# Kernel tuning notes

Measured on AMD Instinct MI355X. Metric: run time of the kernel, lower is better.

Reference implementation:

```python
import jax, jax.numpy as jnp
import numpy as np

N = 50000   # nodes
E = 800000  # edges (avg degree 16)
F = 64      # num_features (channels per irrep)
R = 8       # radial basis size
H = 64      # radial MLP hidden
S = 10      # num_species
NPATH = 5   # tensor-product paths: s*Y0->0, s*Y1->1, v*Y0->1, v.Y1->0, v x Y1->1
AVG_NEIGH = 16.0


def setup_inputs() -> dict:
    key = jax.random.key(0)
    ks = jax.random.split(key, 20)
    def w(k, shape, fan_in):
        return jax.random.normal(k, shape, dtype=jnp.float32) / np.sqrt(fan_in)
    return dict(
        vectors=jax.random.normal(ks[0], (E, 3), dtype=jnp.float32),
        node_feats_s=jax.random.normal(ks[1], (N, F), dtype=jnp.float32),
        node_feats_v=jax.random.normal(ks[2], (N, F, 3), dtype=jnp.float32),
        radial_embedding=jax.random.normal(ks[3], (E, R), dtype=jnp.float32),
        Wu_s=w(ks[7], (F, F), F), Wu_v=w(ks[8], (F, F), F),
        W_r1=w(ks[9], (R, H), R), W_r2=w(ks[10], (H, NPATH * F), H),
        Wd_s=w(ks[11], (F, F), F), Wd_v=w(ks[12], (F, F), F),
        w_sym_s=jax.random.normal(ks[13], (S, 3, F), dtype=jnp.float32),
        w_sym_v=jax.random.normal(ks[14], (S, 2, F), dtype=jnp.float32),
        WL_s=w(ks[15], (F, F), F), WL_v=w(ks[16], (F, F), F),
        W_skip_s=w(ks[17], (S, F, F), F), W_skip_v=w(ks[18], (S, F, F), F),
        W_out=w(ks[19], (F, 1), F),
        node_specie=jax.random.randint(ks[4], (N,), 0, S),
        senders=jax.random.randint(ks[5], (E,), 0, N),
        receivers=jax.random.randint(ks[6], (E,), 0, N),
    )


def reference(vectors, node_feats_s, node_feats_v, radial_embedding,
              Wu_s, Wu_v, W_r1, W_r2, Wd_s, Wd_v,
              w_sym_s, w_sym_v, WL_s, WL_v, W_skip_s, W_skip_v, W_out,
              node_specie, senders, receivers):
    n = node_feats_s.shape[0]
    # ---- self-connection: species-indexed linear (skip_tp), per-irrep channel mix
    sc_s = jnp.einsum('nf,nfg->ng', node_feats_s, W_skip_s[node_specie])
    sc_v = jnp.einsum('nfc,nfg->ngc', node_feats_v, W_skip_v[node_specie])
    # ---- InteractionBlock: linear up
    s = node_feats_s @ Wu_s                                  # [N,F]
    v = jnp.einsum('nfc,fg->ngc', node_feats_v, Wu_v)        # [N,F,3]
    # radial MLP -> per-edge, per-path, per-channel tensor-product weights
    h = jax.nn.silu(radial_embedding @ W_r1)
    w = (h @ W_r2).reshape(-1, NPATH, s.shape[1])            # [E,5,F]
    # spherical harmonics (l=1): unit edge vectors
    Y1 = vectors / (jnp.linalg.norm(vectors, axis=-1, keepdims=True) + 1e-9)  # [E,3]
    xs = s[senders]                                          # [E,F]
    xv = v[senders]                                          # [E,F,3]
    # CG tensor product paths (0e+1o) x (Y0+Y1) -> 0e + 1o
    m_s = w[:, 0] * xs + w[:, 3] * jnp.einsum('efc,ec->ef', xv, Y1)
    m_v = (w[:, 1, :, None] * xs[:, :, None] * Y1[:, None, :]
           + w[:, 2, :, None] * xv
           + w[:, 4, :, None] * jnp.cross(xv, Y1[:, None, :]))
    # scatter-sum aggregation over receivers
    agg_s = jax.ops.segment_sum(m_s, receivers, num_segments=n)
    agg_v = jax.ops.segment_sum(m_v, receivers, num_segments=n)
    # linear down to num_features * interaction_irreps
    s = agg_s @ Wd_s
    v = jnp.einsum('nfc,fg->ngc', agg_v, Wd_v)
    # epsilon is None -> divide by sqrt(avg_num_neighbors)
    inv = 1.0 / np.sqrt(AVG_NEIGH).astype(np.float32)
    s = s * inv
    v = v * inv
    # ---- EquivariantProductBasisBlock: symmetric contraction (correlation=2),
    # species-indexed per-channel weights over the symmetric CG basis
    ws = w_sym_s[node_specie]                                # [N,3,F]
    wv = w_sym_v[node_specie]                                # [N,2,F]
    ps = ws[:, 0] * s + ws[:, 1] * s * s + ws[:, 2] * jnp.sum(v * v, axis=-1)
    pv = wv[:, 0, :, None] * v + wv[:, 1, :, None] * (s[:, :, None] * v)
    # linear to num_features * hidden_irreps
    fs = ps @ WL_s
    fv = jnp.einsum('nfc,fg->ngc', pv, WL_v)
    # residual skip connection
    fs = fs + sc_s
    fv = fv + sc_v
    # ---- LinearReadoutBlock to output_irreps = '0e'
    node_outputs = fs @ W_out                                # [N,1]
    return node_outputs, fs, fv
```

## Files before the change

kernel.cpp:

```cpp
#include <hip/hip_runtime.h>
#include <stdint.h>

#define F 64
#define RDIM 8
#define HDIM 64
#define NPATH 5
#define EB 64
#define PADH 72
#define PADN 324
#define NSP 16
#define PB 72
#define NT 4

typedef _Float16 half8 __attribute__((ext_vector_type(8)));
typedef _Float16 half4 __attribute__((ext_vector_type(4)));
typedef float floatx4 __attribute__((ext_vector_type(4)));

__device__ inline half8 h8_from_f32(const float* p) {
    float4 a = ((const float4*)p)[0];
    float4 b = ((const float4*)p)[1];
    half8 h;
    h[0] = (_Float16)a.x; h[1] = (_Float16)a.y; h[2] = (_Float16)a.z; h[3] = (_Float16)a.w;
    h[4] = (_Float16)b.x; h[5] = (_Float16)b.y; h[6] = (_Float16)b.z; h[7] = (_Float16)b.w;
    return h;
}

__device__ inline half8 h8_from_f32_stride3(const float* p) {
    half8 h;
#pragma unroll
    for (int j = 0; j < 8; ++j) h[j] = (_Float16)p[j * 3];
    return h;
}

__device__ inline half8 h8_zero() {
    half8 h;
#pragma unroll
    for (int j = 0; j < 8; ++j) h[j] = (_Float16)0.f;
    return h;
}

__global__ __launch_bounds__(256) void k_pre_mfma(
    const float* __restrict__ nfs, const float* __restrict__ nfv,
    const float* __restrict__ Wus, const float* __restrict__ Wuv,
    half4* __restrict__ comb, int N)
{
    __shared__ _Float16 BT[2][64 * PB];
    const int tid = threadIdx.x;
    const int wave = tid >> 6, lane = tid & 63;
    const int l15 = lane & 15, lq = lane >> 4;
    const int tb0 = blockIdx.x * 64;

    {
        const float* srcs[2] = { Wus, Wuv };
#pragma unroll
        for (int m = 0; m < 2; ++m) {
            const float* W = srcs[m];
#pragma unroll
            for (int rep = 0; rep < 16; ++rep) {
                int id = rep * 256 + tid;
                int k = id >> 6, n = id & 63;
                BT[m][n * PB + k] = (_Float16)W[k * F + n];
            }
        }
    }
    __syncthreads();

    const int tb = tb0 + wave * 16;
    const int ndA = tb + l15;

#define BFRAG(m, nt, ks) (*(const half8*)&BT[m][((nt) * 16 + l15) * PB + (ks) * 32 + lq * 8])

    floatx4 c[4][NT];
#pragma unroll
    for (int q = 0; q < 4; ++q)
#pragma unroll
        for (int nt = 0; nt < NT; ++nt) c[q][nt] = (floatx4){0.f, 0.f, 0.f, 0.f};

#pragma unroll
    for (int ks = 0; ks < 2; ++ks) {
        half8 a_s, a_v0, a_v1, a_v2;
        if (ndA < N) {
            a_s  = h8_from_f32(nfs + (size_t)ndA * F + ks * 32 + lq * 8);
            const float* vb = nfv + ((size_t)ndA * F + ks * 32 + lq * 8) * 3;
            a_v0 = h8_from_f32_stride3(vb + 0);
            a_v1 = h8_from_f32_stride3(vb + 1);
            a_v2 = h8_from_f32_stride3(vb + 2);
        } else {
            a_s = a_v0 = a_v1 = a_v2 = h8_zero();
        }
#pragma unroll
        for (int nt = 0; nt < NT; ++nt) {
            half8 bs = BFRAG(0, nt, ks);
            half8 bv = BFRAG(1, nt, ks);
            c[0][nt] = __builtin_amdgcn_mfma_f32_16x16x32_f16(a_s,  bs, c[0][nt], 0, 0, 0);
            c[1][nt] = __builtin_amdgcn_mfma_f32_16x16x32_f16(a_v0, bv, c[1][nt], 0, 0, 0);
            c[2][nt] = __builtin_amdgcn_mfma_f32_16x16x32_f16(a_v1, bv, c[2][nt], 0, 0, 0);
            c[3][nt] = __builtin_amdgcn_mfma_f32_16x16x32_f16(a_v2, bv, c[3][nt], 0, 0, 0);
        }
    }
#undef BFRAG

#pragma unroll
    for (int r = 0; r < 4; ++r) {
        const int nd = tb + lq * 4 + r;
        if (nd < N) {
#pragma unroll
            for (int nt = 0; nt < NT; ++nt) {
                half4 o;
                o[0] = (_Float16)c[0][nt][r];
                o[1] = (_Float16)c[1][nt][r];
                o[2] = (_Float16)c[2][nt][r];
                o[3] = (_Float16)c[3][nt][r];
                comb[(size_t)nd * F + nt * 16 + l15] = o;
            }
        }
    }
}

__global__ __launch_bounds__(256) void k_hist(
    const int* __restrict__ recv, int* __restrict__ cnt, int E,
    const int* __restrict__ specie, int* __restrict__ nbin, int N)
{
    __shared__ int lbin[NSP];
    const int tid = threadIdx.x;
    if (tid < NSP) lbin[tid] = 0;
    __syncthreads();
    const int i0 = blockIdx.x * 256 + tid;
    const int stride = gridDim.x * 256;
    for (int e = i0; e < E; e += stride) atomicAdd(&cnt[recv[e]], 1);
    for (int n = i0; n < N; n += stride) atomicAdd(&lbin[specie[n]], 1);
    __syncthreads();
    if (tid < NSP && lbin[tid] > 0) atomicAdd(&nbin[tid], lbin[tid]);
}

__global__ __launch_bounds__(1024) void k_scanA(
    const int* __restrict__ cnt, int* __restrict__ bsum, int N)
{
    __shared__ int lsum[1024];
    const int tid = threadIdx.x;
    const int i = blockIdx.x * 1024 + tid;
    int x = (i < N) ? cnt[i] : 0;
    lsum[tid] = x;
    __syncthreads();
    for (int off = 512; off > 0; off >>= 1) {
        if (tid < off) lsum[tid] += lsum[tid + off];
        __syncthreads();
    }
    if (tid == 0) bsum[blockIdx.x] = lsum[0];
}

__global__ __launch_bounds__(64) void k_scanB(
    int* __restrict__ bsum, int nb,
    const int* __restrict__ nbin, int* __restrict__ ncur)
{
    const int lane = threadIdx.x;
    int carry = 0;
    for (int base = 0; base < nb; base += 64) {
        const int idx = base + lane;
        int v = (idx < nb) ? bsum[idx] : 0;
        int incl = v;
#pragma unroll
        for (int off = 1; off < 64; off <<= 1) {
            int u = __shfl_up(incl, off, 64);
            if (lane >= off) incl += u;
        }
        int tot = __shfl(incl, 63, 64);
        if (idx < nb) bsum[idx] = incl - v + carry;
        carry += tot;
    }
    if (lane == 0) {
        int run = 0;
        for (int s = 0; s < NSP; ++s) {
            ncur[s] = run;
            run += ((nbin[s] + 63) >> 6) << 6;
        }
    }
}

__global__ __launch_bounds__(1024) void k_scanC(
    const int* __restrict__ cnt, const int* __restrict__ bsum,
    int* __restrict__ cursor, int N)
{
    __shared__ int lsum[1024];
    const int tid = threadIdx.x;
    const int i = blockIdx.x * 1024 + tid;
    int x = (i < N) ? cnt[i] : 0;
    lsum[tid] = x;
    __syncthreads();
    int acc = x;
    for (int off = 1; off < 1024; off <<= 1) {
        int add = (tid >= off) ? lsum[tid - off] : 0;
        __syncthreads();
        acc += add;
        lsum[tid] = acc;
        __syncthreads();
    }
    if (i < N) cursor[i] = acc - x + bsum[blockIdx.x];
}

__global__ __launch_bounds__(256) void k_scatter(
    const int* __restrict__ recv, const int* __restrict__ send,
    int* __restrict__ cursor, int* __restrict__ perm,
    int2* __restrict__ srsort, int E,
    const int* __restrict__ specie, int* __restrict__ ncur,
    int* __restrict__ nperm, int N)
{
    __shared__ int lbin[NSP], lbase[NSP], lcur[NSP];
    const int tid = threadIdx.x;
    const int i0 = blockIdx.x * 256 + tid;
    const int stride = gridDim.x * 256;
    for (int e = i0; e < E; e += stride) {
        int r = recv[e];
        int p = atomicAdd(&cursor[r], 1);
        perm[p] = e;
        srsort[p] = make_int2(send[e], r);
    }
    if (tid < NSP) { lbin[tid] = 0; lcur[tid] = 0; }
    __syncthreads();
    int sp = -1;
    if (i0 < N) { sp = specie[i0]; atomicAdd(&lbin[sp], 1); }
    __syncthreads();
    if (tid < NSP && lbin[tid] > 0) lbase[tid] = atomicAdd(&ncur[tid], lbin[tid]);
    __syncthreads();
    if (i0 < N) {
        int off = atomicAdd(&lcur[sp], 1);
        nperm[lbase[sp] + off] = i0;
    }
}

__global__ __launch_bounds__(256, 3) void k_edge(
    const float* __restrict__ vecs, const float* __restrict__ re,
    const float* __restrict__ Wr1, const float* __restrict__ Wr2,
    const int* __restrict__ perm, const int2* __restrict__ srsort,
    const half4* __restrict__ comb,
    float* __restrict__ agg_s, float* __restrict__ agg_v, int E)
{
    __shared__ _Float16 h_lds[EB * PADH];
    __shared__ _Float16 w_lds[EB * PADN];
    const int tid = threadIdx.x;
    const int wave = tid >> 6, lane = tid & 63;
    const int l15 = lane & 15, lq = lane >> 4;

    half8 bfrag[5][2];
#pragma unroll
    for (int nt = 0; nt < 5; ++nt)
#pragma unroll
        for (int ks = 0; ks < 2; ++ks)
#pragma unroll
            for (int j = 0; j < 8; ++j) {
                int k = ks * 32 + lq * 8 + j;
                int n = wave * 80 + nt * 16 + l15;
                bfrag[nt][ks][j] = (_Float16)Wr2[k * (NPATH * F) + n];
            }

    float w1r[RDIM];
#pragma unroll
    for (int r = 0; r < RDIM; ++r) w1r[r] = Wr1[r * HDIM + lane];

    const int niter = (E + EB - 1) / EB;
    for (int it = blockIdx.x; it < niter; it += gridDim.x) {
        const int base = it * EB;
        const bool full = (base + EB <= E);

        if (full) {
            const int ew = base + wave * 16;
            int pm[16];
#pragma unroll
            for (int j = 0; j < 4; ++j)
                ((int4*)pm)[j] = ((const int4*)(perm + ew))[j];
            float4 ra[4], rb[4];
#pragma unroll
            for (int j = 0; j < 4; ++j) {
                const float4* rp = (const float4*)(re + (size_t)pm[j] * RDIM);
                ra[j] = rp[0]; rb[j] = rp[1];
            }
#pragma unroll
            for (int t = 0; t < 16; ++t) {
                float4 A = ra[t & 3], B = rb[t & 3];
                if (t < 12) {
                    const float4* rp = (const float4*)(re + (size_t)pm[t + 4] * RDIM);
                    ra[t & 3] = rp[0]; rb[t & 3] = rp[1];
                }
                float h = A.x * w1r[0] + A.y * w1r[1] + A.z * w1r[2] + A.w * w1r[3]
                        + B.x * w1r[4] + B.y * w1r[5] + B.z * w1r[6] + B.w * w1r[7];
                h = h / (1.f + __expf(-h));
                h_lds[(wave * 16 + t) * PADH + lane] = (_Float16)h;
            }
        } else {
            for (int t = 0; t < 16; ++t) {
                const int eloc = wave * 16 + t;
                const int e = base + eloc;
                float h = 0.f;
                if (e < E) {
                    const int pe = perm[e];
                    const float4* rp = (const float4*)(re + (size_t)pe * RDIM);
                    float4 A = rp[0], B = rp[1];
                    h = A.x * w1r[0] + A.y * w1r[1] + A.z * w1r[2] + A.w * w1r[3]
                      + B.x * w1r[4] + B.y * w1r[5] + B.z * w1r[6] + B.w * w1r[7];
                    h = h / (1.f + __expf(-h));
                }
                h_lds[eloc * PADH + lane] = (_Float16)h;
            }
        }
        __syncthreads();

        floatx4 c[4][5];
#pragma unroll
        for (int mt = 0; mt < 4; ++mt)
#pragma unroll
            for (int nt = 0; nt < 5; ++nt)
                c[mt][nt] = (floatx4){0.f, 0.f, 0.f, 0.f};
#pragma unroll
        for (int ks = 0; ks < 2; ++ks) {
            half8 a[4];
#pragma unroll
            for (int mt = 0; mt < 4; ++mt)
                a[mt] = *(const half8*)&h_lds[(mt * 16 + l15) * PADH + ks * 32 + lq * 8];
#pragma unroll
            for (int mt = 0; mt < 4; ++mt)
#pragma unroll
                for (int nt = 0; nt < 5; ++nt)
                    c[mt][nt] = __builtin_amdgcn_mfma_f32_16x16x32_f16(
                        a[mt], bfrag[nt][ks], c[mt][nt], 0, 0, 0);
        }
#pragma unroll
        for (int mt = 0; mt < 4; ++mt)
#pragma unroll
            for (int nt = 0; nt < 5; ++nt)
#pragma unroll
                for (int r = 0; r < 4; ++r) {
                    int row = mt * 16 + lq * 4 + r;
                    int col = wave * 80 + nt * 16 + l15;
                    w_lds[row * PADN + col] = (_Float16)c[mt][nt][r];
                }
        __syncthreads();

        if (full) {
            const int ew = base + wave * 16;
            int pm[16];
            int2 sr[16];
#pragma unroll
            for (int j = 0; j < 4; ++j)
                ((int4*)pm)[j] = ((const int4*)(perm + ew))[j];
#pragma unroll
            for (int j = 0; j < 8; ++j)
                ((int4*)sr)[j] = ((const int4*)(srsort + ew))[j];
            half4 gb[4];
            float vxr[4], vyr[4], vzr[4];
#pragma unroll
            for (int j = 0; j < 4; ++j) {
                gb[j] = comb[(size_t)sr[j].x * F + lane];
                const float* vp = vecs + (size_t)pm[j] * 3;
                vxr[j] = vp[0]; vyr[j] = vp[1]; vzr[j] = vp[2];
            }
            float accs = 0.f, acc0 = 0.f, acc1 = 0.f, acc2 = 0.f;
            int cur = sr[0].y;
#pragma unroll
            for (int t = 0; t < 16; ++t) {
                half4 g = gb[t & 3];
                float vx = vxr[t & 3], vy = vyr[t & 3], vz = vzr[t & 3];
                if (t < 12) {
                    gb[t & 3] = comb[(size_t)sr[t + 4].x * F + lane];
                    const float* vp = vecs + (size_t)pm[t + 4] * 3;
                    vxr[t & 3] = vp[0]; vyr[t & 3] = vp[1]; vzr[t & 3] = vp[2];
                }
                const int eloc = wave * 16 + t;
                float nrm = sqrtf(vx * vx + vy * vy + vz * vz);
                float inv = 1.f / (nrm + 1e-9f);
                float Yx = vx * inv, Yy = vy * inv, Yz = vz * inv;
                float w0  = (float)w_lds[eloc * PADN + 0 * F + lane];
                float w1p = (float)w_lds[eloc * PADN + 1 * F + lane];
                float w2p = (float)w_lds[eloc * PADN + 2 * F + lane];
                float w3p = (float)w_lds[eloc * PADN + 3 * F + lane];
                float w4p = (float)w_lds[eloc * PADN + 4 * F + lane];
                float xs = (float)g[0], x0 = (float)g[1], x1 = (float)g[2], x2 = (float)g[3];
                float dvY = x0 * Yx + x1 * Yy + x2 * Yz;
                float ms = w0 * xs + w3p * dvY;
                float m0 = w1p * xs * Yx + w2p * x0 + w4p * (x1 * Yz - x2 * Yy);
                float m1 = w1p * xs * Yy + w2p * x1 + w4p * (x2 * Yx - x0 * Yz);
                float m2 = w1p * xs * Yz + w2p * x2 + w4p * (x0 * Yy - x1 * Yx);
                if (sr[t].y != cur) {
                    float* asb = agg_s + (size_t)cur * F;
                    float* avb = agg_v + (size_t)cur * 3 * F;
                    unsafeAtomicAdd(&asb[lane], accs);
                    unsafeAtomicAdd(&avb[lane], acc0);
                    unsafeAtomicAdd(&avb[F + lane], acc1);
                    unsafeAtomicAdd(&avb[2 * F + lane], acc2);
                    accs = acc0 = acc1 = acc2 = 0.f;
                    cur = sr[t].y;
                }
                accs += ms; acc0 += m0; acc1 += m1; acc2 += m2;
            }
            {
                float* asb = agg_s + (size_t)cur * F;
                float* avb = agg_v + (size_t)cur * 3 * F;
                unsafeAtomicAdd(&asb[lane], accs);
                unsafeAtomicAdd(&avb[lane], acc0);
                unsafeAtomicAdd(&avb[F + lane], acc1);
                unsafeAtomicAdd(&avb[2 * F + lane], acc2);
            }
        } else {
            for (int t = 0; t < 16; ++t) {
                const int eloc = wave * 16 + t;
                const int e = base + eloc;
                if (e >= E) break;
                const int pe = perm[e];
                const int2 sr = srsort[e];
                const int snd = sr.x, rcv = sr.y;
                const float* vp = vecs + (size_t)pe * 3;
                float vx = vp[0], vy = vp[1], vz = vp[2];
                float nrm = sqrtf(vx * vx + vy * vy + vz * vz);
                float inv = 1.f / (nrm + 1e-9f);
                float Yx = vx * inv, Yy = vy * inv, Yz = vz * inv;
                half4 g = comb[(size_t)snd * F + lane];
                float w0  = (float)w_lds[eloc * PADN + 0 * F + lane];
                float w1p = (float)w_lds[eloc * PADN + 1 * F + lane];
                float w2p = (float)w_lds[eloc * PADN + 2 * F + lane];
                float w3p = (float)w_lds[eloc * PADN + 3 * F + lane];
                float w4p = (float)w_lds[eloc * PADN + 4 * F + lane];
                float xs = (float)g[0], x0 = (float)g[1], x1 = (float)g[2], x2 = (float)g[3];
                float dvY = x0 * Yx + x1 * Yy + x2 * Yz;
                float ms = w0 * xs + w3p * dvY;
                float m0 = w1p * xs * Yx + w2p * x0 + w4p * (x1 * Yz - x2 * Yy);
                float m1 = w1p * xs * Yy + w2p * x1 + w4p * (x2 * Yx - x0 * Yz);
                float m2 = w1p * xs * Yz + w2p * x2 + w4p * (x0 * Yy - x1 * Yx);
                float* asb = agg_s + (size_t)rcv * F;
                float* avb = agg_v + (size_t)rcv * 3 * F;
                unsafeAtomicAdd(&asb[lane], ms);
                unsafeAtomicAdd(&avb[lane], m0);
                unsafeAtomicAdd(&avb[F + lane], m1);
                unsafeAtomicAdd(&avb[2 * F + lane], m2);
            }
        }
    }
}

__global__ __launch_bounds__(256) void k_post_mfma(
    const float* __restrict__ agg_s, const float* __restrict__ agg_v,
    const float* __restrict__ nfs, const float* __restrict__ nfv,
    const float* __restrict__ Wds, const float* __restrict__ Wdv,
    const float* __restrict__ wss, const float* __restrict__ wsv,
    const float* __restrict__ WLs, const float* __restrict__ WLv,
    const float* __restrict__ Wsks, const float* __restrict__ Wskv,
    const float* __restrict__ Wout, const int* __restrict__ specie,
    const int* __restrict__ nperm,
    float* __restrict__ out0, float* __restrict__ out_fs,
    float* __restrict__ out_fv, int N)
{
    __shared__ _Float16 BT[6][64 * PB];
    __shared__ _Float16 P_lds[4][16 * PB];
    const int tid = threadIdx.x;
    const int wave = tid >> 6, lane = tid & 63;
    const int l15 = lane & 15, lq = lane >> 4;
    const int tb0 = blockIdx.x * 64;

    const int nfirst = nperm[tb0];
    const int sp = (nfirst < 0) ? 0 : specie[nfirst];

    {
        const float* srcs[6] = { Wds, Wdv,
                                 Wsks + (size_t)sp * F * F, Wskv + (size_t)sp * F * F,
                                 WLs, WLv };
#pragma unroll
        for (int m = 0; m < 6; ++m) {
            const float* W = srcs[m];
#pragma unroll
            for (int rep = 0; rep < 16; ++rep) {
                int id = rep * 256 + tid;
                int k = id >> 6, n = id & 63;
                BT[m][n * PB + k] = (_Float16)W[k * F + n];
            }
        }
    }
    __syncthreads();

    const int tb = tb0 + wave * 16;
    const int ndA = nperm[tb + l15];
    int ndr[4];
#pragma unroll
    for (int r = 0; r < 4; ++r) ndr[r] = nperm[tb + lq * 4 + r];

#define BFRAG(m, nt, ks) (*(const half8*)&BT[m][((nt) * 16 + l15) * PB + (ks) * 32 + lq * 8])

    floatx4 csk[4][NT];
#pragma unroll
    for (int q = 0; q < 4; ++q)
#pragma unroll
        for (int nt = 0; nt < NT; ++nt) csk[q][nt] = (floatx4){0.f, 0.f, 0.f, 0.f};
#pragma unroll
    for (int ks = 0; ks < 2; ++ks) {
        half8 a_s, a_v0, a_v1, a_v2;
        if (ndA >= 0) {
            a_s  = h8_from_f32(nfs + (size_t)ndA * F + ks * 32 + lq * 8);
            const float* vb = nfv + ((size_t)ndA * F + ks * 32 + lq * 8) * 3;
            a_v0 = h8_from_f32_stride3(vb + 0);
            a_v1 = h8_from_f32_stride3(vb + 1);
            a_v2 = h8_from_f32_stride3(vb + 2);
        } else {
            a_s = a_v0 = a_v1 = a_v2 = h8_zero();
        }
#pragma unroll
        for (int nt = 0; nt < NT; ++nt) {
            half8 bs = BFRAG(2, nt, ks);
            half8 bv = BFRAG(3, nt, ks);
            csk[0][nt] = __builtin_amdgcn_mfma_f32_16x16x32_f16(a_s,  bs, csk[0][nt], 0, 0, 0);
            csk[1][nt] = __builtin_amdgcn_mfma_f32_16x16x32_f16(a_v0, bv, csk[1][nt], 0, 0, 0);
            csk[2][nt] = __builtin_amdgcn_mfma_f32_16x16x32_f16(a_v1, bv, csk[2][nt], 0, 0, 0);
            csk[3][nt] = __builtin_amdgcn_mfma_f32_16x16x32_f16(a_v2, bv, csk[3][nt], 0, 0, 0);
        }
    }

    floatx4 cdn[4][NT];
#pragma unroll
    for (int q = 0; q < 4; ++q)
#pragma unroll
        for (int nt = 0; nt < NT; ++nt) cdn[q][nt] = (floatx4){0.f, 0.f, 0.f, 0.f};
#pragma unroll
    for (int ks = 0; ks < 2; ++ks) {
        half8 a_s, a_v0, a_v1, a_v2;
        if (ndA >= 0) {
            a_s  = h8_from_f32(agg_s + (size_t)ndA * F + ks * 32 + lq * 8);
            const float* vb = agg_v + (size_t)ndA * 3 * F + ks * 32 + lq * 8;
            a_v0 = h8_from_f32(vb);
            a_v1 = h8_from_f32(vb + F);
            a_v2 = h8_from_f32(vb + 2 * F);
        } else {
            a_s = a_v0 = a_v1 = a_v2 = h8_zero();
        }
#pragma unroll
        for (int nt = 0; nt < NT; ++nt) {
            half8 bs = BFRAG(0, nt, ks);
            half8 bv = BFRAG(1, nt, ks);
            cdn[0][nt] = __builtin_amdgcn_mfma_f32_16x16x32_f16(a_s,  bs, cdn[0][nt], 0, 0, 0);
            cdn[1][nt] = __builtin_amdgcn_mfma_f32_16x16x32_f16(a_v0, bv, cdn[1][nt], 0, 0, 0);
            cdn[2][nt] = __builtin_amdgcn_mfma_f32_16x16x32_f16(a_v1, bv, cdn[2][nt], 0, 0, 0);
            cdn[3][nt] = __builtin_amdgcn_mfma_f32_16x16x32_f16(a_v2, bv, cdn[3][nt], 0, 0, 0);
        }
    }

#pragma unroll
    for (int nt = 0; nt < NT; ++nt) {
        const int g = nt * 16 + l15;
        float a0 = wss[(sp * 3 + 0) * F + g];
        float a1 = wss[(sp * 3 + 1) * F + g];
        float a2 = wss[(sp * 3 + 2) * F + g];
        float b0 = wsv[(sp * 2 + 0) * F + g];
        float b1 = wsv[(sp * 2 + 1) * F + g];
#pragma unroll
        for (int r = 0; r < 4; ++r) {
            const float inv = 0.25f;
            float s2  = cdn[0][nt][r] * inv;
            float v20 = cdn[1][nt][r] * inv;
            float v21 = cdn[2][nt][r] * inv;
            float v22 = cdn[3][nt][r] * inv;
            cdn[0][nt][r] = a0 * s2 + a1 * s2 * s2
                          + a2 * (v20 * v20 + v21 * v21 + v22 * v22);
            cdn[1][nt][r] = b0 * v20 + b1 * s2 * v20;
            cdn[2][nt][r] = b0 * v21 + b1 * s2 * v21;
            cdn[3][nt][r] = b0 * v22 + b1 * s2 * v22;
        }
    }

#pragma unroll
    for (int q = 0; q < 4; ++q) {
#pragma unroll
        for (int nt = 0; nt < NT; ++nt)
#pragma unroll
            for (int r = 0; r < 4; ++r)
                P_lds[wave][(lq * 4 + r) * PB + nt * 16 + l15] = (_Float16)cdn[q][nt][r];
        __syncthreads();
        half8 ap0 = *(const half8*)&P_lds[wave][l15 * PB + 0 * 32 + lq * 8];
        half8 ap1 = *(const half8*)&P_lds[wave][l15 * PB + 1 * 32 + lq * 8];
        const int bm = (q == 0) ? 4 : 5;
#pragma unroll
        for (int nt = 0; nt < NT; ++nt) {
            csk[q][nt] = __builtin_amdgcn_mfma_f32_16x16x32_f16(ap0, BFRAG(bm, nt, 0), csk[q][nt], 0, 0, 0);
            csk[q][nt] = __builtin_amdgcn_mfma_f32_16x16x32_f16(ap1, BFRAG(bm, nt, 1), csk[q][nt], 0, 0, 0);
        }
        __syncthreads();
    }
#undef BFRAG

    float wo[NT];
#pragma unroll
    for (int nt = 0; nt < NT; ++nt) wo[nt] = Wout[nt * 16 + l15];
#pragma unroll
    for (int r = 0; r < 4; ++r) {
        const int nd = ndr[r];
        float po = 0.f;
        if (nd >= 0) {
#pragma unroll
            for (int nt = 0; nt < NT; ++nt) {
                const int g = nt * 16 + l15;
                float fs = csk[0][nt][r];
                out_fs[(size_t)nd * F + g] = fs;
                po += fs * wo[nt];
                float* fvp = out_fv + ((size_t)nd * F + g) * 3;
                fvp[0] = csk[1][nt][r];
                fvp[1] = csk[2][nt][r];
                fvp[2] = csk[3][nt][r];
            }
            po += __shfl_xor(po, 1, 64);
            po += __shfl_xor(po, 2, 64);
            po += __shfl_xor(po, 4, 64);
            po += __shfl_xor(po, 8, 64);
            if (l15 == 0) out0[nd] = po;
        }
    }
}

extern "C" void kernel_launch(void* const* d_in, const int* in_sizes, int n_in,
                              void* d_out, int out_size, void* d_ws, size_t ws_size,
                              hipStream_t stream)
{
    const float* vectors = (const float*)d_in[0];
    const float* nfs  = (const float*)d_in[1];
    const float* nfv  = (const float*)d_in[2];
    const float* re   = (const float*)d_in[3];
    const float* Wus  = (const float*)d_in[4];
    const float* Wuv  = (const float*)d_in[5];
    const float* Wr1  = (const float*)d_in[6];
    const float* Wr2  = (const float*)d_in[7];
    const float* Wds  = (const float*)d_in[8];
    const float* Wdv  = (const float*)d_in[9];
    const float* wss  = (const float*)d_in[10];
    const float* wsv  = (const float*)d_in[11];
    const float* WLs  = (const float*)d_in[12];
    const float* WLv  = (const float*)d_in[13];
    const float* Wsks = (const float*)d_in[14];
    const float* Wskv = (const float*)d_in[15];
    const float* Wout = (const float*)d_in[16];
    const int* specie    = (const int*)d_in[17];
    const int* senders   = (const int*)d_in[18];
    const int* receivers = (const int*)d_in[19];

    const int N = in_sizes[1] / F;
    const int E = in_sizes[18];

    const size_t NF = (size_t)N * F;
    const int NPAD_MAX = N + NSP * 64 + 64;
    half4* comb  = (half4*)d_ws;
    float* agg_s = (float*)((char*)d_ws + NF * sizeof(half4));
    float* agg_v = agg_s + NF;
    int*   perm  = (int*)(agg_v + 3 * NF);
    int2*  srsort = (int2*)(perm + E);
    int*   cnt    = (int*)(srsort + E);
    int*   nbin   = cnt + N;
    int*   ncur   = nbin + NSP;
    int*   cursor = ncur + NSP;
    int*   bsum   = cursor + N;
    int*   nperm  = bsum + 64;

    hipMemsetAsync(agg_s, 0, (size_t)4 * NF * sizeof(float), stream);
    hipMemsetAsync(cnt, 0, (size_t)(N + NSP) * sizeof(int), stream);
    hipMemsetAsync(nperm, 0xFF, (size_t)NPAD_MAX * sizeof(int), stream);

    const int nb64 = (N + 63) / 64;
    const int nbs = (N + 1023) / 1024;
    const int nbp = (N + NSP * 64 + 63) / 64;

    k_pre_mfma<<<nb64, 256, 0, stream>>>(nfs, nfv, Wus, Wuv, comb, N);
    k_hist<<<1024, 256, 0, stream>>>(receivers, cnt, E, specie, nbin, N);
    k_scanA<<<nbs, 1024, 0, stream>>>(cnt, bsum, N);
    k_scanB<<<1, 64, 0, stream>>>(bsum, nbs, nbin, ncur);
    k_scanC<<<nbs, 1024, 0, stream>>>(cnt, bsum, cursor, N);
    k_scatter<<<1024, 256, 0, stream>>>(receivers, senders, cursor,
                                        perm, srsort, E, specie, ncur, nperm, N);
    k_edge<<<2048, 256, 0, stream>>>(vectors, re, Wr1, Wr2, perm, srsort,
                                     comb, agg_s, agg_v, E);
    float* out0   = (float*)d_out;
    float* out_fs = out0 + N;
    float* out_fv = out_fs + (size_t)N * F;
    k_post_mfma<<<nbp, 256, 0, stream>>>(agg_s, agg_v, nfs, nfv, Wds, Wdv,
                                         wss, wsv, WLs, WLv, Wsks, Wskv,
                                         Wout, specie, nperm,
                                         out0, out_fs, out_fv, N);
}
```

Before: 551.9 us.

## Halve edge block size, pack sorted edge metadata into int4, raise occupancy

Edge tiles shrink from 64 to 32 edges per block (8 per wave), which cuts LDS use and accumulator registers so the launch bound can rise from 3 to 6 blocks per CU. The separate perm and sender/receiver arrays are merged into a single 16-byte record per edge, written with a nontemporal store and read once into registers, which removes the duplicate index loads. The grid grows to 2500 blocks. In exchange the MFMA work per barrier halves, the prefetch depth per wave is shorter, and runs of the same receiver split more often, so there may be more atomics.

```diff
diff --git a/kernel.cpp b/kernel.cpp
--- a/kernel.cpp
+++ b/kernel.cpp
@@ -5,7 +5,8 @@
 #define RDIM 8
 #define HDIM 64
 #define NPATH 5
-#define EB 64
+#define EB 32
+#define EPW 8
 #define PADH 72
 #define PADN 324
 #define NSP 16
@@ -15,6 +16,7 @@
 typedef _Float16 half8 __attribute__((ext_vector_type(8)));
 typedef _Float16 half4 __attribute__((ext_vector_type(4)));
 typedef float floatx4 __attribute__((ext_vector_type(4)));
+typedef int intx4 __attribute__((ext_vector_type(4)));
 
 __device__ inline half8 h8_from_f32(const float* p) {
     float4 a = ((const float4*)p)[0];
@@ -200,8 +202,7 @@
 
 __global__ __launch_bounds__(256) void k_scatter(
     const int* __restrict__ recv, const int* __restrict__ send,
-    int* __restrict__ cursor, int* __restrict__ perm,
-    int2* __restrict__ srsort, int E,
+    int* __restrict__ cursor, intx4* __restrict__ esort, int E,
     const int* __restrict__ specie, int* __restrict__ ncur,
     int* __restrict__ nperm, int N)
 {
@@ -212,8 +213,8 @@
     for (int e = i0; e < E; e += stride) {
         int r = recv[e];
         int p = atomicAdd(&cursor[r], 1);
-        perm[p] = e;
-        srsort[p] = make_int2(send[e], r);
+        intx4 v = (intx4){e, send[e], r, 0};
+        __builtin_nontemporal_store(v, &esort[p]);
     }
     if (tid < NSP) { lbin[tid] = 0; lcur[tid] = 0; }
     __syncthreads();
@@ -228,10 +229,10 @@
     }
 }
 
-__global__ __launch_bounds__(256, 3) void k_edge(
+__global__ __launch_bounds__(256, 6) void k_edge(
     const float* __restrict__ vecs, const float* __restrict__ re,
     const float* __restrict__ Wr1, const float* __restrict__ Wr2,
-    const int* __restrict__ perm, const int2* __restrict__ srsort,
+    const intx4* __restrict__ esort,
     const half4* __restrict__ comb,
     float* __restrict__ agg_s, float* __restrict__ agg_v, int E)
 {
@@ -261,38 +262,37 @@
     for (int it = blockIdx.x; it < niter; it += gridDim.x) {
         const int base = it * EB;
         const bool full = (base + EB <= E);
+        intx4 es[EPW];
 
         if (full) {
-            const int ew = base + wave * 16;
-            int pm[16];
-#pragma unroll
-            for (int j = 0; j < 4; ++j)
-                ((int4*)pm)[j] = ((const int4*)(perm + ew))[j];
+            const int ew = base + wave * EPW;
+#pragma unroll
+            for (int j = 0; j < EPW; ++j) es[j] = esort[ew + j];
             float4 ra[4], rb[4];
 #pragma unroll
             for (int j = 0; j < 4; ++j) {
-                const float4* rp = (const float4*)(re + (size_t)pm[j] * RDIM);
+                const float4* rp = (const float4*)(re + (size_t)es[j].x * RDIM);
                 ra[j] = rp[0]; rb[j] = rp[1];
             }
 #pragma unroll
-            for (int t = 0; t < 16; ++t) {
+            for (int t = 0; t < EPW; ++t) {
                 float4 A = ra[t & 3], B = rb[t & 3];
-                if (t < 12) {
-                    const float4* rp = (const float4*)(re + (size_t)pm[t + 4] * RDIM);
+                if (t < EPW - 4) {
+                    const float4* rp = (const float4*)(re + (size_t)es[t + 4].x * RDIM);
                     ra[t & 3] = rp[0]; rb[t & 3] = rp[1];
                 }
                 float h = A.x * w1r[0] + A.y * w1r[1] + A.z * w1r[2] + A.w * w1r[3]
                         + B.x * w1r[4] + B.y * w1r[5] + B.z * w1r[6] + B.w * w1r[7];
                 h = h / (1.f + __expf(-h));
-                h_lds[(wave * 16 + t) * PADH + lane] = (_Float16)h;
+                h_lds[(wave * EPW + t) * PADH + lane] = (_Float16)h;
             }
         } else {
-            for (int t = 0; t < 16; ++t) {
-                const int eloc = wave * 16 + t;
+            for (int t = 0; t < EPW; ++t) {
+                const int eloc = wave * EPW + t;
                 const int e = base + eloc;
                 float h = 0.f;
                 if (e < E) {
-                    const int pe = perm[e];
+                    const int pe = esort[e].x;
                     const float4* rp = (const float4*)(re + (size_t)pe * RDIM);
                     float4 A = rp[0], B = rp[1];
                     h = A.x * w1r[0] + A.y * w1r[1] + A.z * w1r[2] + A.w * w1r[3]
@@ -304,27 +304,27 @@
         }
         __syncthreads();
 
-        floatx4 c[4][5];
-#pragma unroll
-        for (int mt = 0; mt < 4; ++mt)
+        floatx4 c[2][5];
+#pragma unroll
+        for (int mt = 0; mt < 2; ++mt)
 #pragma unroll
             for (int nt = 0; nt < 5; ++nt)
                 c[mt][nt] = (floatx4){0.f, 0.f, 0.f, 0.f};
 #pragma unroll
         for (int ks = 0; ks < 2; ++ks) {
-            half8 a[4];
-#pragma unroll
-            for (int mt = 0; mt < 4; ++mt)
+            half8 a[2];
+#pragma unroll
+            for (int mt = 0; mt < 2; ++mt)
                 a[mt] = *(const half8*)&h_lds[(mt * 16 + l15) * PADH + ks * 32 + lq * 8];
 #pragma unroll
-            for (int mt = 0; mt < 4; ++mt)
+            for (int mt = 0; mt < 2; ++mt)
 #pragma unroll
                 for (int nt = 0; nt < 5; ++nt)
                     c[mt][nt] = __builtin_amdgcn_mfma_f32_16x16x32_f16(
                         a[mt], bfrag[nt][ks], c[mt][nt], 0, 0, 0);
         }
 #pragma unroll
-        for (int mt = 0; mt < 4; ++mt)
+        for (int mt = 0; mt < 2; ++mt)
 #pragma unroll
             for (int nt = 0; nt < 5; ++nt)
 #pragma unroll
@@ -336,35 +336,26 @@
         __syncthreads();
 
         if (full) {
-            const int ew = base + wave * 16;
-            int pm[16];
-            int2 sr[16];
-#pragma unroll
-            for (int j = 0; j < 4; ++j)
-                ((int4*)pm)[j] = ((const int4*)(perm + ew))[j];
-#pragma unroll
-            for (int j = 0; j < 8; ++j)
-                ((int4*)sr)[j] = ((const int4*)(srsort + ew))[j];
             half4 gb[4];
             float vxr[4], vyr[4], vzr[4];
 #pragma unroll
             for (int j = 0; j < 4; ++j) {
-                gb[j] = comb[(size_t)sr[j].x * F + lane];
-                const float* vp = vecs + (size_t)pm[j] * 3;
+                gb[j] = comb[(size_t)es[j].y * F + lane];
+                const float* vp = vecs + (size_t)es[j].x * 3;
                 vxr[j] = vp[0]; vyr[j] = vp[1]; vzr[j] = vp[2];
             }
             float accs = 0.f, acc0 = 0.f, acc1 = 0.f, acc2 = 0.f;
-            int cur = sr[0].y;
-#pragma unroll
-            for (int t = 0; t < 16; ++t) {
+            int cur = es[0].z;
+#pragma unroll
+            for (int t = 0; t < EPW; ++t) {
                 half4 g = gb[t & 3];
                 float vx = vxr[t & 3], vy = vyr[t & 3], vz = vzr[t & 3];
-                if (t < 12) {
-                    gb[t & 3] = comb[(size_t)sr[t + 4].x * F + lane];
-                    const float* vp = vecs + (size_t)pm[t + 4] * 3;
+                if (t < EPW - 4) {
+                    gb[t & 3] = comb[(size_t)es[t + 4].y * F + lane];
+                    const float* vp = vecs + (size_t)es[t + 4].x * 3;
                     vxr[t & 3] = vp[0]; vyr[t & 3] = vp[1]; vzr[t & 3] = vp[2];
                 }
-                const int eloc = wave * 16 + t;
+                const int eloc = wave * EPW + t;
                 float nrm = sqrtf(vx * vx + vy * vy + vz * vz);
                 float inv = 1.f / (nrm + 1e-9f);
                 float Yx = vx * inv, Yy = vy * inv, Yz = vz * inv;
@@ -379,7 +370,7 @@
                 float m0 = w1p * xs * Yx + w2p * x0 + w4p * (x1 * Yz - x2 * Yy);
                 float m1 = w1p * xs * Yy + w2p * x1 + w4p * (x2 * Yx - x0 * Yz);
                 float m2 = w1p * xs * Yz + w2p * x2 + w4p * (x0 * Yy - x1 * Yx);
-                if (sr[t].y != cur) {
+                if (es[t].z != cur) {
                     float* asb = agg_s + (size_t)cur * F;
                     float* avb = agg_v + (size_t)cur * 3 * F;
                     unsafeAtomicAdd(&asb[lane], accs);
@@ -387,7 +378,7 @@
                     unsafeAtomicAdd(&avb[F + lane], acc1);
                     unsafeAtomicAdd(&avb[2 * F + lane], acc2);
                     accs = acc0 = acc1 = acc2 = 0.f;
-                    cur = sr[t].y;
+                    cur = es[t].z;
                 }
                 accs += ms; acc0 += m0; acc1 += m1; acc2 += m2;
             }
@@ -400,13 +391,12 @@
                 unsafeAtomicAdd(&avb[2 * F + lane], acc2);
             }
         } else {
-            for (int t = 0; t < 16; ++t) {
-                const int eloc = wave * 16 + t;
+            for (int t = 0; t < EPW; ++t) {
+                const int eloc = wave * EPW + t;
                 const int e = base + eloc;
                 if (e >= E) break;
-                const int pe = perm[e];
-                const int2 sr = srsort[e];
-                const int snd = sr.x, rcv = sr.y;
+                const intx4 sr = esort[e];
+                const int pe = sr.x, snd = sr.y, rcv = sr.z;
                 const float* vp = vecs + (size_t)pe * 3;
                 float vx = vp[0], vy = vp[1], vz = vp[2];
                 float nrm = sqrtf(vx * vx + vy * vy + vz * vz);
@@ -642,9 +632,8 @@
     half4* comb  = (half4*)d_ws;
     float* agg_s = (float*)((char*)d_ws + NF * sizeof(half4));
     float* agg_v = agg_s + NF;
-    int*   perm  = (int*)(agg_v + 3 * NF);
-    int2*  srsort = (int2*)(perm + E);
-    int*   cnt    = (int*)(srsort + E);
+    intx4* esort = (intx4*)(agg_v + 3 * NF);
+    int*   cnt    = (int*)(esort + E);
     int*   nbin   = cnt + N;
     int*   ncur   = nbin + NSP;
     int*   cursor = ncur + NSP;
@@ -665,8 +654,8 @@
     k_scanB<<<1, 64, 0, stream>>>(bsum, nbs, nbin, ncur);
     k_scanC<<<nbs, 1024, 0, stream>>>(cnt, bsum, cursor, N);
     k_scatter<<<1024, 256, 0, stream>>>(receivers, senders, cursor,
-                                        perm, srsort, E, specie, ncur, nperm, N);
-    k_edge<<<2048, 256, 0, stream>>>(vectors, re, Wr1, Wr2, perm, srsort,
+                                        esort, E, specie, ncur, nperm, N);
+    k_edge<<<2500, 256, 0, stream>>>(vectors, re, Wr1, Wr2, esort,
                                      comb, agg_s, agg_v, E);
     float* out0   = (float*)d_out;
     float* out_fs = out0 + N;
```

After: 1.040 ms. +88.4%, slower.
